# Kernel optimization log

Hardware: AMD Instinct MI355X
Metric: run time of the kernel (lower is better)

The kernel has to match this reference:

```python
import jax, jax.numpy as jnp
from jax import lax
import numpy as np

NUM_TOKENS = 14
DIM = 512
B, T = 32, 512


def _lstm(xs, W_ih, W_hh, b_ih, b_hh):
    """PyTorch-semantics single-layer LSTM, batch_first. xs: [B,T,D] -> hs: [B,T,D].
    Gate order i, f, g, o; gates = x @ W_ih^T + b_ih + h @ W_hh^T + b_hh."""
    Bsz, Tlen, D = xs.shape
    # Precompute input contribution for all timesteps (one big GEMM).
    pre = jnp.einsum('btd,gd->btg', xs, W_ih) + (b_ih + b_hh)  # [B,T,4D]

    def step(carry, p):
        h, c = carry
        gates = p + h @ W_hh.T  # [B,4D]
        i, f, g, o = jnp.split(gates, 4, axis=-1)
        i = jax.nn.sigmoid(i)
        f = jax.nn.sigmoid(f)
        g = jnp.tanh(g)
        o = jax.nn.sigmoid(o)
        c = f * c + i * g
        h = o * jnp.tanh(c)
        return (h, c), h

    h0 = jnp.zeros((Bsz, D), xs.dtype)
    (_, _), hs = lax.scan(step, (h0, h0), jnp.swapaxes(pre, 0, 1))  # time-major scan
    return jnp.swapaxes(hs, 0, 1)  # [B,T,D]


def setup_inputs() -> dict:
    key = jax.random.key(0)
    ks = jax.random.split(key, 10)
    s_emb = 1.0  # nn.Embedding default init N(0,1)
    s = 1.0 / np.sqrt(DIM)  # nn.LSTM default init U(-1/sqrt(H), 1/sqrt(H))
    u = lambda k, shape: jax.random.uniform(k, shape, jnp.float32, -s, s)
    return {
        'x': jax.random.randint(ks[0], (B, T), 0, NUM_TOKENS, dtype=jnp.int32),
        'embed': jax.random.normal(ks[1], (NUM_TOKENS, DIM), jnp.float32) * s_emb,
        'W_ih_q': u(ks[2], (4 * DIM, DIM)),
        'W_hh_q': u(ks[3], (4 * DIM, DIM)),
        'b_ih_q': u(ks[4], (4 * DIM,)),
        'b_hh_q': u(ks[5], (4 * DIM,)),
        'W_ih_k': u(ks[6], (4 * DIM, DIM)),
        'W_hh_k': u(ks[7], (4 * DIM, DIM)),
        'b_ih_k': u(ks[8], (4 * DIM,)),
        'b_hh_k': u(ks[9], (4 * DIM,)),
    }


def reference(x, embed, W_ih_q, W_hh_q, b_ih_q, b_hh_q, W_ih_k, W_hh_k, b_ih_k, b_hh_k):
    e = embed[x]  # [B,T,D] embedding lookup
    q = _lstm(e, W_ih_q, W_hh_q, b_ih_q, b_hh_q)  # [B,T,D]
    k = _lstm(e, W_ih_k, W_hh_k, b_ih_k, b_hh_k)  # [B,T,D]
    A = jnp.einsum('btd,bsd->bts', q, k)  # bmm(q, k^T) -> [B,T,T]
    return A
```

## Files before the change

### kernel.cpp

```cpp
#include <hip/hip_runtime.h>
#include <hip/hip_bf16.h>


#define TB 32
#define TT 512
#define TD 512
#define NTOK 14

typedef __attribute__((ext_vector_type(8))) short short8;
typedef __attribute__((ext_vector_type(4))) float f32x4;

__device__ __forceinline__ float fsigmoid(float v) { return 1.f / (1.f + __expf(-v)); }
__device__ __forceinline__ float ftanh(float v) {
    float a = fabsf(v);
    float e = __expf(-2.f * a);
    float r = (1.f - e) / (1.f + e);
    return copysignf(r, v);
}
__device__ __forceinline__ unsigned int f2bf(float f) {
    __hip_bfloat16 h = __float2bfloat16(f);
    return (unsigned int)__builtin_bit_cast(unsigned short, h);
}

__device__ __forceinline__ short8 load16_coh(const unsigned short* p) {
    short8 r;
    asm volatile("global_load_dwordx4 %0, %1, off sc0 sc1" : "=v"(r) : "v"(p));
    return r;
}
__device__ __forceinline__ void store2_coh(unsigned short* p, unsigned int v) {
    asm volatile("global_store_short %0, %1, off sc0 sc1" :: "v"(p), "v"(v) : "memory");
}
__device__ __forceinline__ void store4_coh(unsigned int* p, unsigned int v) {
    asm volatile("global_store_dword %0, %1, off sc0 sc1" :: "v"(p), "v"(v) : "memory");
}
__device__ __forceinline__ unsigned int load4_coh(const unsigned int* p) {
    unsigned int r;
    asm volatile("global_load_dword %0, %1, off sc0 sc1\n\ts_waitcnt vmcnt(0)"
                 : "=v"(r) : "v"(p) : "memory");
    return r;
}

__global__ __launch_bounds__(256) void pre_tab_kernel(
    const float* __restrict__ embed,
    const float* __restrict__ Wih_q, const float* __restrict__ bih_q, const float* __restrict__ bhh_q,
    const float* __restrict__ Wih_k, const float* __restrict__ bih_k, const float* __restrict__ bhh_k,
    float* __restrict__ pre)
{
    int idx = blockIdx.x * 256 + threadIdx.x;
    int l = idx / (NTOK * 4 * TD);
    int r = idx % (NTOK * 4 * TD);
    int tok = r / (4 * TD), j = r % (4 * TD);
    const float* Wih = l ? Wih_k : Wih_q;
    float acc = l ? (bih_k[j] + bhh_k[j]) : (bih_q[j] + bhh_q[j]);
    const float4* e4 = (const float4*)(embed + (size_t)tok * TD);
    const float4* w4 = (const float4*)(Wih + (size_t)j * TD);
    for (int t2 = 0; t2 < TD / 4; ++t2) {
        float4 e = e4[t2], w = w4[t2];
        acc += e.x * w.x + e.y * w.y + e.z * w.z + e.w * w.w;
    }
    pre[idx] = acc;
}

__global__ void init_flags(unsigned int* flags) { flags[threadIdx.x] = 0; }

__global__ __launch_bounds__(256) void lstm_persist(
    const float* __restrict__ Whh_q, const float* __restrict__ Whh_k,
    const float* __restrict__ pre,
    const int* __restrict__ x,
    float* __restrict__ qout, float* __restrict__ kout,
    unsigned short* __restrict__ hbf,
    unsigned int* __restrict__ flags)
{
    __shared__ unsigned short w_lds[64][512];
    __shared__ unsigned short h_lds[16][512];
    __shared__ float          g_lds[64][17];
    __shared__ unsigned char  x_lds[16 * TT];
    __shared__ float          pre_lds[NTOK][64];

    int wg  = blockIdx.x;
    int l   = wg >> 6;
    int g   = (wg >> 5) & 1;
    int wid = wg & 31;
    int d0  = wid << 4;
    int tid = threadIdx.x;
    int lane = tid & 63;
    int rt  = tid >> 6;

    const float* Whh = l ? Whh_k : Whh_q;
    float* hist = l ? kout : qout;
    unsigned short* hb_l = hbf + (size_t)l * 2 * TB * TD;
    unsigned int* fl = flags + (l * 2 + g) * 32;

    {
        int r = tid >> 2;
        const float* src = Whh + (size_t)((r >> 4) * TD + d0 + (r & 15)) * TD;
#pragma unroll
        for (int i = 0; i < 16; ++i) {
            int c = (tid & 3) + 4 * i;
            float4 a = ((const float4*)src)[c * 2];
            float4 b4 = ((const float4*)src)[c * 2 + 1];
            unsigned short* dst = &w_lds[r][(c ^ (r & 7)) * 8];
            dst[0] = (unsigned short)f2bf(a.x); dst[1] = (unsigned short)f2bf(a.y);
            dst[2] = (unsigned short)f2bf(a.z); dst[3] = (unsigned short)f2bf(a.w);
            dst[4] = (unsigned short)f2bf(b4.x); dst[5] = (unsigned short)f2bf(b4.y);
            dst[6] = (unsigned short)f2bf(b4.z); dst[7] = (unsigned short)f2bf(b4.w);
        }
    }
    for (int i = tid; i < 16 * TT; i += 256)
        x_lds[i] = (unsigned char)x[(g * 16 + (i >> 9)) * TT + (i & 511)];
    for (int i = tid; i < NTOK * 64; i += 256) {
        int tok = i >> 6, j = i & 63;
        pre_lds[tok][j] = pre[((size_t)l * NTOK + tok) * (4 * TD) + (j >> 4) * TD + d0 + (j & 15)];
    }
    __syncthreads();

    int bl = tid >> 4, dd = tid & 15;
    int bg = g * 16 + bl;
    float creg = 0.f;

    {
        int tok = x_lds[bl * TT];
        float i_ = fsigmoid(pre_lds[tok][dd]);
        float f_ = fsigmoid(pre_lds[tok][16 + dd]);
        float g_ = ftanh(pre_lds[tok][32 + dd]);
        float o_ = fsigmoid(pre_lds[tok][48 + dd]);
        creg = i_ * g_;
        float h = o_ * ftanh(creg);
        store2_coh(hb_l + (size_t)bg * TD + d0 + dd, f2bf(h));
        hist[((size_t)bg * TT) * TD + d0 + dd] = h;
        asm volatile("s_waitcnt vmcnt(0)" ::: "memory");
    }
    __syncthreads();
    if (tid == 0) store4_coh(fl + wid, 1u);

    for (int t = 1; t < TT; ++t) {
        {
            unsigned int need = (unsigned int)t;
            for (;;) {
                unsigned int v = load4_coh(fl + (lane & 31));
                if (__all((int)(v >= need))) break;
                __builtin_amdgcn_s_sleep(1);
            }
        }
        {
            int row = tid >> 4;
            const unsigned short* hb = hb_l + (size_t)((t - 1) & 1) * TB * TD
                                            + (size_t)(g * 16 + row) * TD;
            short8 v0 = load16_coh(hb + ((tid & 15) +  0) * 8);
            short8 v1 = load16_coh(hb + ((tid & 15) + 16) * 8);
            short8 v2 = load16_coh(hb + ((tid & 15) + 32) * 8);
            short8 v3 = load16_coh(hb + ((tid & 15) + 48) * 8);
            asm volatile("s_waitcnt vmcnt(0)" ::: "memory");
            __builtin_amdgcn_sched_barrier(0);
            *(short8*)&h_lds[row][(((tid & 15) +  0) ^ (row & 7)) * 8] = v0;
            *(short8*)&h_lds[row][(((tid & 15) + 16) ^ (row & 7)) * 8] = v1;
            *(short8*)&h_lds[row][(((tid & 15) + 32) ^ (row & 7)) * 8] = v2;
            *(short8*)&h_lds[row][(((tid & 15) + 48) ^ (row & 7)) * 8] = v3;
        }
        __syncthreads();

        {
            f32x4 acc = {0.f, 0.f, 0.f, 0.f};
            int rr = rt * 16 + (lane & 15);
            int hr = lane & 15;
#pragma unroll
            for (int kk = 0; kk < 16; ++kk) {
                int c = kk * 4 + (lane >> 4);
                short8 a  = *(const short8*)&h_lds[hr][(c ^ (hr & 7)) * 8];
                short8 bf = *(const short8*)&w_lds[rr][(c ^ (rr & 7)) * 8];
                acc = __builtin_amdgcn_mfma_f32_16x16x32_bf16(a, bf, acc, 0, 0, 0);
            }
            int gb = (lane >> 4) << 2;
#pragma unroll
            for (int r2 = 0; r2 < 4; ++r2) g_lds[rr][gb + r2] = acc[r2];
        }
        __syncthreads();

        {
            int tok = x_lds[bl * TT + t];
            float gi = g_lds[dd][bl]      + pre_lds[tok][dd];
            float gf = g_lds[16 + dd][bl] + pre_lds[tok][16 + dd];
            float gg = g_lds[32 + dd][bl] + pre_lds[tok][32 + dd];
            float go = g_lds[48 + dd][bl] + pre_lds[tok][48 + dd];
            float i_ = fsigmoid(gi), f_ = fsigmoid(gf), g2 = ftanh(gg), o_ = fsigmoid(go);
            creg = f_ * creg + i_ * g2;
            float h = o_ * ftanh(creg);
            store2_coh(hb_l + (size_t)(t & 1) * TB * TD + (size_t)bg * TD + d0 + dd, f2bf(h));
            hist[((size_t)bg * TT + t) * TD + d0 + dd] = h;
            asm volatile("s_waitcnt vmcnt(0)" ::: "memory");
        }
        __syncthreads();
        if (tid == 0) store4_coh(fl + wid, (unsigned int)(t + 1));
    }
}

__global__ __launch_bounds__(256) void qk_gemm(
    const float* __restrict__ q, const float* __restrict__ k, float* __restrict__ A)
{
    __shared__ float qs[64][68];
    __shared__ float ks[64][68];
    int b = blockIdx.y;
    int t0 = (blockIdx.x >> 3) * 64;
    int s0 = (blockIdx.x & 7) * 64;
    const float* qb = q + (size_t)b * TT * TD;
    const float* kb = k + (size_t)b * TT * TD;
    int tid = threadIdx.x;
    int ty = tid >> 4, tx = tid & 15;
    float accr[4][4] = {};
    for (int k0 = 0; k0 < TD; k0 += 64) {
        for (int i = tid; i < 64 * 16; i += 256) {
            int r = i >> 4, c4 = i & 15;
            ((float4*)&qs[r][0])[c4] = ((const float4*)(qb + (size_t)(t0 + r) * TD + k0))[c4];
            ((float4*)&ks[r][0])[c4] = ((const float4*)(kb + (size_t)(s0 + r) * TD + k0))[c4];
        }
        __syncthreads();
#pragma unroll 4
        for (int kk = 0; kk < 64; kk += 4) {
            float4 qv[4], kv[4];
#pragma unroll
            for (int i = 0; i < 4; ++i) qv[i] = *(const float4*)&qs[ty * 4 + i][kk];
#pragma unroll
            for (int j = 0; j < 4; ++j) kv[j] = *(const float4*)&ks[tx * 4 + j][kk];
#pragma unroll
            for (int i = 0; i < 4; ++i)
#pragma unroll
                for (int j = 0; j < 4; ++j)
                    accr[i][j] += qv[i].x * kv[j].x + qv[i].y * kv[j].y
                                + qv[i].z * kv[j].z + qv[i].w * kv[j].w;
        }
        __syncthreads();
    }
    for (int i = 0; i < 4; ++i)
        for (int j = 0; j < 4; ++j)
            A[(size_t)b * TT * TT + (size_t)(t0 + ty * 4 + i) * TT + (s0 + tx * 4 + j)] = accr[i][j];
}

extern "C" void kernel_launch(void* const* d_in, const int* in_sizes, int n_in,
                              void* d_out, int out_size, void* d_ws, size_t ws_size,
                              hipStream_t stream)
{
    const int*   x      = (const int*)d_in[0];
    const float* embed  = (const float*)d_in[1];
    const float* Wih_q  = (const float*)d_in[2];
    const float* Whh_q  = (const float*)d_in[3];
    const float* bih_q  = (const float*)d_in[4];
    const float* bhh_q  = (const float*)d_in[5];
    const float* Wih_k  = (const float*)d_in[6];
    const float* Whh_k  = (const float*)d_in[7];
    const float* bih_k  = (const float*)d_in[8];
    const float* bhh_k  = (const float*)d_in[9];

    float* ws   = (float*)d_ws;
    float* q    = ws;
    float* kbuf = q + (size_t)TB * TT * TD;
    float* pre  = kbuf + (size_t)TB * TT * TD;
    unsigned short* hbf = (unsigned short*)(pre + 2 * NTOK * 4 * TD);
    unsigned int* flags = (unsigned int*)(hbf + 65536);

    init_flags<<<1, 128, 0, stream>>>(flags);
    pre_tab_kernel<<<224, 256, 0, stream>>>(embed, Wih_q, bih_q, bhh_q,
                                            Wih_k, bih_k, bhh_k, pre);
    lstm_persist<<<128, 256, 0, stream>>>(Whh_q, Whh_k, pre, x, q, kbuf, hbf, flags);
    dim3 g2(64, 32);
    qk_gemm<<<g2, 256, 0, stream>>>(q, kbuf, (float*)d_out);
}
```

Baseline: 1.651 ms.

## Interleave two batch halves per workgroup to overlap flag waits with compute

Each persistent LSTM workgroup now handles both 16-row batch halves instead of one, halving the grid to 64 workgroups. The two halves are ping-ponged: while one half's MFMA and gate math run, the h-state loads and flag polling for the other half are in flight. This hides inter-workgroup synchronization latency on the serial recurrence. The cost is twice the per-workgroup compute on the critical path, fewer CUs in use, and more intricate flag ordering that could deadlock or race if wrong.

```diff
diff --git a/kernel.cpp b/kernel.cpp
--- a/kernel.cpp
+++ b/kernel.cpp
@@ -74,12 +74,11 @@
     __shared__ unsigned short w_lds[64][512];
     __shared__ unsigned short h_lds[16][512];
     __shared__ float          g_lds[64][17];
-    __shared__ unsigned char  x_lds[16 * TT];
+    __shared__ unsigned char  x_lds[TB * TT];
     __shared__ float          pre_lds[NTOK][64];
 
     int wg  = blockIdx.x;
-    int l   = wg >> 6;
-    int g   = (wg >> 5) & 1;
+    int l   = wg >> 5;
     int wid = wg & 31;
     int d0  = wid << 4;
     int tid = threadIdx.x;
@@ -89,7 +88,8 @@
     const float* Whh = l ? Whh_k : Whh_q;
     float* hist = l ? kout : qout;
     unsigned short* hb_l = hbf + (size_t)l * 2 * TB * TD;
-    unsigned int* fl = flags + (l * 2 + g) * 32;
+    unsigned int* flA = flags + (l * 2 + 0) * 32;
+    unsigned int* flB = flags + (l * 2 + 1) * 32;
 
     {
         int r = tid >> 2;
@@ -106,8 +106,7 @@
             dst[6] = (unsigned short)f2bf(b4.z); dst[7] = (unsigned short)f2bf(b4.w);
         }
     }
-    for (int i = tid; i < 16 * TT; i += 256)
-        x_lds[i] = (unsigned char)x[(g * 16 + (i >> 9)) * TT + (i & 511)];
+    for (int i = tid; i < TB * TT; i += 256) x_lds[i] = (unsigned char)x[i];
     for (int i = tid; i < NTOK * 64; i += 256) {
         int tok = i >> 6, j = i & 63;
         pre_lds[tok][j] = pre[((size_t)l * NTOK + tok) * (4 * TD) + (j >> 4) * TD + d0 + (j & 15)];
@@ -115,49 +114,72 @@
     __syncthreads();
 
     int bl = tid >> 4, dd = tid & 15;
-    int bg = g * 16 + bl;
-    float creg = 0.f;
+    int row = tid >> 4;
+    float cregA = 0.f, cregB = 0.f;
 
     {
-        int tok = x_lds[bl * TT];
-        float i_ = fsigmoid(pre_lds[tok][dd]);
-        float f_ = fsigmoid(pre_lds[tok][16 + dd]);
-        float g_ = ftanh(pre_lds[tok][32 + dd]);
-        float o_ = fsigmoid(pre_lds[tok][48 + dd]);
-        creg = i_ * g_;
-        float h = o_ * ftanh(creg);
-        store2_coh(hb_l + (size_t)bg * TD + d0 + dd, f2bf(h));
-        hist[((size_t)bg * TT) * TD + d0 + dd] = h;
+        int tokA = x_lds[bl * TT];
+        float iA = fsigmoid(pre_lds[tokA][dd]);
+        float fA = fsigmoid(pre_lds[tokA][16 + dd]);
+        float gA = ftanh(pre_lds[tokA][32 + dd]);
+        float oA = fsigmoid(pre_lds[tokA][48 + dd]);
+        cregA = iA * gA;
+        float hA = oA * ftanh(cregA);
+        store2_coh(hb_l + (size_t)bl * TD + d0 + dd, f2bf(hA));
+        hist[((size_t)bl * TT) * TD + d0 + dd] = hA;
+        int tokB = x_lds[(16 + bl) * TT];
+        float iB = fsigmoid(pre_lds[tokB][dd]);
+        float fB = fsigmoid(pre_lds[tokB][16 + dd]);
+        float gB = ftanh(pre_lds[tokB][32 + dd]);
+        float oB = fsigmoid(pre_lds[tokB][48 + dd]);
+        cregB = iB * gB;
+        float hB = oB * ftanh(cregB);
+        store2_coh(hb_l + (size_t)(16 + bl) * TD + d0 + dd, f2bf(hB));
+        hist[((size_t)(16 + bl) * TT) * TD + d0 + dd] = hB;
         asm volatile("s_waitcnt vmcnt(0)" ::: "memory");
     }
     __syncthreads();
-    if (tid == 0) store4_coh(fl + wid, 1u);
+    if (tid == 0) { store4_coh(flA + wid, 1u); store4_coh(flB + wid, 1u); }
+
+    short8 pA0, pA1, pA2, pA3;
+    {
+        for (;;) {
+            unsigned int v = load4_coh(flA + (lane & 31));
+            if (__all((int)(v >= 1u))) break;
+            __builtin_amdgcn_s_sleep(1);
+        }
+        const unsigned short* hb = hb_l + (size_t)row * TD;
+        pA0 = load16_coh(hb + ((tid & 15) +  0) * 8);
+        pA1 = load16_coh(hb + ((tid & 15) + 16) * 8);
+        pA2 = load16_coh(hb + ((tid & 15) + 32) * 8);
+        pA3 = load16_coh(hb + ((tid & 15) + 48) * 8);
+    }
 
     for (int t = 1; t < TT; ++t) {
+        asm volatile("s_waitcnt vmcnt(0)" ::: "memory");
+        __builtin_amdgcn_sched_barrier(0);
+        *(short8*)&h_lds[row][(((tid & 15) +  0) ^ (row & 7)) * 8] = pA0;
+        *(short8*)&h_lds[row][(((tid & 15) + 16) ^ (row & 7)) * 8] = pA1;
+        *(short8*)&h_lds[row][(((tid & 15) + 32) ^ (row & 7)) * 8] = pA2;
+        *(short8*)&h_lds[row][(((tid & 15) + 48) ^ (row & 7)) * 8] = pA3;
+        __syncthreads();
+        if (tid == 0 && t >= 2) store4_coh(flB + wid, (unsigned int)t);
+
+        short8 pB0, pB1, pB2, pB3;
         {
             unsigned int need = (unsigned int)t;
             for (;;) {
-                unsigned int v = load4_coh(fl + (lane & 31));
+                unsigned int v = load4_coh(flB + (lane & 31));
                 if (__all((int)(v >= need))) break;
                 __builtin_amdgcn_s_sleep(1);
             }
-        }
-        {
-            int row = tid >> 4;
             const unsigned short* hb = hb_l + (size_t)((t - 1) & 1) * TB * TD
-                                            + (size_t)(g * 16 + row) * TD;
-            short8 v0 = load16_coh(hb + ((tid & 15) +  0) * 8);
-            short8 v1 = load16_coh(hb + ((tid & 15) + 16) * 8);
-            short8 v2 = load16_coh(hb + ((tid & 15) + 32) * 8);
-            short8 v3 = load16_coh(hb + ((tid & 15) + 48) * 8);
-            asm volatile("s_waitcnt vmcnt(0)" ::: "memory");
-            __builtin_amdgcn_sched_barrier(0);
-            *(short8*)&h_lds[row][(((tid & 15) +  0) ^ (row & 7)) * 8] = v0;
-            *(short8*)&h_lds[row][(((tid & 15) + 16) ^ (row & 7)) * 8] = v1;
-            *(short8*)&h_lds[row][(((tid & 15) + 32) ^ (row & 7)) * 8] = v2;
-            *(short8*)&h_lds[row][(((tid & 15) + 48) ^ (row & 7)) * 8] = v3;
-        }
-        __syncthreads();
+                                            + (size_t)(16 + row) * TD;
+            pB0 = load16_coh(hb + ((tid & 15) +  0) * 8);
+            pB1 = load16_coh(hb + ((tid & 15) + 16) * 8);
+            pB2 = load16_coh(hb + ((tid & 15) + 32) * 8);
+            pB3 = load16_coh(hb + ((tid & 15) + 48) * 8);
+        }
 
         {
             f32x4 acc = {0.f, 0.f, 0.f, 0.f};
@@ -183,14 +205,64 @@
             float gg = g_lds[32 + dd][bl] + pre_lds[tok][32 + dd];
             float go = g_lds[48 + dd][bl] + pre_lds[tok][48 + dd];
             float i_ = fsigmoid(gi), f_ = fsigmoid(gf), g2 = ftanh(gg), o_ = fsigmoid(go);
-            creg = f_ * creg + i_ * g2;
-            float h = o_ * ftanh(creg);
-            store2_coh(hb_l + (size_t)(t & 1) * TB * TD + (size_t)bg * TD + d0 + dd, f2bf(h));
-            hist[((size_t)bg * TT + t) * TD + d0 + dd] = h;
-            asm volatile("s_waitcnt vmcnt(0)" ::: "memory");
-        }
-        __syncthreads();
-        if (tid == 0) store4_coh(fl + wid, (unsigned int)(t + 1));
+            cregA = f_ * cregA + i_ * g2;
+            float h = o_ * ftanh(cregA);
+            store2_coh(hb_l + (size_t)(t & 1) * TB * TD + (size_t)bl * TD + d0 + dd, f2bf(h));
+            hist[((size_t)bl * TT + t) * TD + d0 + dd] = h;
+        }
+
+        asm volatile("s_waitcnt vmcnt(0)" ::: "memory");
+        __builtin_amdgcn_sched_barrier(0);
+        *(short8*)&h_lds[row][(((tid & 15) +  0) ^ (row & 7)) * 8] = pB0;
+        *(short8*)&h_lds[row][(((tid & 15) + 16) ^ (row & 7)) * 8] = pB1;
+        *(short8*)&h_lds[row][(((tid & 15) + 32) ^ (row & 7)) * 8] = pB2;
+        *(short8*)&h_lds[row][(((tid & 15) + 48) ^ (row & 7)) * 8] = pB3;
+        __syncthreads();
+        if (tid == 0) store4_coh(flA + wid, (unsigned int)(t + 1));
+
+        if (t < TT - 1) {
+            unsigned int need = (unsigned int)(t + 1);
+            for (;;) {
+                unsigned int v = load4_coh(flA + (lane & 31));
+                if (__all((int)(v >= need))) break;
+                __builtin_amdgcn_s_sleep(1);
+            }
+            const unsigned short* hb = hb_l + (size_t)(t & 1) * TB * TD + (size_t)row * TD;
+            pA0 = load16_coh(hb + ((tid & 15) +  0) * 8);
+            pA1 = load16_coh(hb + ((tid & 15) + 16) * 8);
+            pA2 = load16_coh(hb + ((tid & 15) + 32) * 8);
+            pA3 = load16_coh(hb + ((tid & 15) + 48) * 8);
+        }
+
+        {
+            f32x4 acc = {0.f, 0.f, 0.f, 0.f};
+            int rr = rt * 16 + (lane & 15);
+            int hr = lane & 15;
+#pragma unroll
+            for (int kk = 0; kk < 16; ++kk) {
+                int c = kk * 4 + (lane >> 4);
+                short8 a  = *(const short8*)&h_lds[hr][(c ^ (hr & 7)) * 8];
+                short8 bf = *(const short8*)&w_lds[rr][(c ^ (rr & 7)) * 8];
+                acc = __builtin_amdgcn_mfma_f32_16x16x32_bf16(a, bf, acc, 0, 0, 0);
+            }
+            int gb = (lane >> 4) << 2;
+#pragma unroll
+            for (int r2 = 0; r2 < 4; ++r2) g_lds[rr][gb + r2] = acc[r2];
+        }
+        __syncthreads();
+
+        {
+            int tok = x_lds[(16 + bl) * TT + t];
+            float gi = g_lds[dd][bl]      + pre_lds[tok][dd];
+            float gf = g_lds[16 + dd][bl] + pre_lds[tok][16 + dd];
+            float gg = g_lds[32 + dd][bl] + pre_lds[tok][32 + dd];
+            float go = g_lds[48 + dd][bl] + pre_lds[tok][48 + dd];
+            float i_ = fsigmoid(gi), f_ = fsigmoid(gf), g2 = ftanh(gg), o_ = fsigmoid(go);
+            cregB = f_ * cregB + i_ * g2;
+            float h = o_ * ftanh(cregB);
+            store2_coh(hb_l + (size_t)(t & 1) * TB * TD + (size_t)(16 + bl) * TD + d0 + dd, f2bf(h));
+            hist[((size_t)(16 + bl) * TT + t) * TD + d0 + dd] = h;
+        }
     }
 }
 
@@ -260,7 +332,7 @@
     init_flags<<<1, 128, 0, stream>>>(flags);
     pre_tab_kernel<<<224, 256, 0, stream>>>(embed, Wih_q, bih_q, bhh_q,
                                             Wih_k, bih_k, bhh_k, pre);
-    lstm_persist<<<128, 256, 0, stream>>>(Whh_q, Whh_k, pre, x, q, kbuf, hbf, flags);
+    lstm_persist<<<64, 256, 0, stream>>>(Whh_q, Whh_k, pre, x, q, kbuf, hbf, flags);
     dim3 g2(64, 32);
     qk_gemm<<<g2, 256, 0, stream>>>(q, kbuf, (float*)d_out);
 }
```

Result: slower. 2.647 ms (+60.3%).

## Use split-bf16 MFMA for QK^T and store LSTM outputs as hi/lo bf16

Applied to the files above, without the earlier changes.

The LSTM kernel now writes each hidden output as a bf16 high part plus a bf16 residual low part instead of fp32. The final Q·K^T batched GEMM is replaced with an MFMA bf16 kernel that runs three products (hh, hl, lh) to approximate fp32 precision. The aim is to move the scalar-FP32 GEMM onto matrix cores and to reduce the store cost of the history writes inside the serial LSTM loop. The trade-off is dropping the lo*lo term, which gives slightly lower precision than fp32, plus three times the MFMA work per product.

```diff
diff --git a/kernel.cpp b/kernel.cpp
--- a/kernel.cpp
+++ b/kernel.cpp
@@ -17,9 +17,13 @@
     float r = (1.f - e) / (1.f + e);
     return copysignf(r, v);
 }
-__device__ __forceinline__ unsigned int f2bf(float f) {
+__device__ __forceinline__ unsigned short f2bf(float f) {
     __hip_bfloat16 h = __float2bfloat16(f);
-    return (unsigned int)__builtin_bit_cast(unsigned short, h);
+    return __builtin_bit_cast(unsigned short, h);
+}
+__device__ __forceinline__ float bf2f(unsigned short u) {
+    unsigned int x = ((unsigned int)u) << 16;
+    return __builtin_bit_cast(float, x);
 }
 
 __device__ __forceinline__ short8 load16_coh(const unsigned short* p) {
@@ -67,7 +71,8 @@
     const float* __restrict__ Whh_q, const float* __restrict__ Whh_k,
     const float* __restrict__ pre,
     const int* __restrict__ x,
-    float* __restrict__ qout, float* __restrict__ kout,
+    unsigned short* __restrict__ qh, unsigned short* __restrict__ ql,
+    unsigned short* __restrict__ kh, unsigned short* __restrict__ kl,
     unsigned short* __restrict__ hbf,
     unsigned int* __restrict__ flags)
 {
@@ -87,7 +92,8 @@
     int rt  = tid >> 6;
 
     const float* Whh = l ? Whh_k : Whh_q;
-    float* hist = l ? kout : qout;
+    unsigned short* hi_arr = l ? kh : qh;
+    unsigned short* lo_arr = l ? kl : ql;
     unsigned short* hb_l = hbf + (size_t)l * 2 * TB * TD;
     unsigned int* fl = flags + (l * 2 + g) * 32;
 
@@ -100,10 +106,10 @@
             float4 a = ((const float4*)src)[c * 2];
             float4 b4 = ((const float4*)src)[c * 2 + 1];
             unsigned short* dst = &w_lds[r][(c ^ (r & 7)) * 8];
-            dst[0] = (unsigned short)f2bf(a.x); dst[1] = (unsigned short)f2bf(a.y);
-            dst[2] = (unsigned short)f2bf(a.z); dst[3] = (unsigned short)f2bf(a.w);
-            dst[4] = (unsigned short)f2bf(b4.x); dst[5] = (unsigned short)f2bf(b4.y);
-            dst[6] = (unsigned short)f2bf(b4.z); dst[7] = (unsigned short)f2bf(b4.w);
+            dst[0] = f2bf(a.x); dst[1] = f2bf(a.y);
+            dst[2] = f2bf(a.z); dst[3] = f2bf(a.w);
+            dst[4] = f2bf(b4.x); dst[5] = f2bf(b4.y);
+            dst[6] = f2bf(b4.z); dst[7] = f2bf(b4.w);
         }
     }
     for (int i = tid; i < 16 * TT; i += 256)
@@ -126,9 +132,12 @@
         float o_ = fsigmoid(pre_lds[tok][48 + dd]);
         creg = i_ * g_;
         float h = o_ * ftanh(creg);
-        store2_coh(hb_l + (size_t)bg * TD + d0 + dd, f2bf(h));
-        hist[((size_t)bg * TT) * TD + d0 + dd] = h;
+        unsigned short hh = f2bf(h);
+        store2_coh(hb_l + (size_t)bg * TD + d0 + dd, hh);
         asm volatile("s_waitcnt vmcnt(0)" ::: "memory");
+        size_t hoff = ((size_t)bg * TT) * TD + d0 + dd;
+        hi_arr[hoff] = hh;
+        lo_arr[hoff] = f2bf(h - bf2f(hh));
     }
     __syncthreads();
     if (tid == 0) store4_coh(fl + wid, 1u);
@@ -185,54 +194,77 @@
             float i_ = fsigmoid(gi), f_ = fsigmoid(gf), g2 = ftanh(gg), o_ = fsigmoid(go);
             creg = f_ * creg + i_ * g2;
             float h = o_ * ftanh(creg);
-            store2_coh(hb_l + (size_t)(t & 1) * TB * TD + (size_t)bg * TD + d0 + dd, f2bf(h));
-            hist[((size_t)bg * TT + t) * TD + d0 + dd] = h;
+            unsigned short hh = f2bf(h);
+            store2_coh(hb_l + (size_t)(t & 1) * TB * TD + (size_t)bg * TD + d0 + dd, hh);
             asm volatile("s_waitcnt vmcnt(0)" ::: "memory");
+            size_t hoff = ((size_t)bg * TT + t) * TD + d0 + dd;
+            hi_arr[hoff] = hh;
+            lo_arr[hoff] = f2bf(h - bf2f(hh));
         }
         __syncthreads();
         if (tid == 0) store4_coh(fl + wid, (unsigned int)(t + 1));
     }
 }
 
-__global__ __launch_bounds__(256) void qk_gemm(
-    const float* __restrict__ q, const float* __restrict__ k, float* __restrict__ A)
+__global__ __launch_bounds__(256) void qk_mfma(
+    const unsigned short* __restrict__ qh, const unsigned short* __restrict__ ql,
+    const unsigned short* __restrict__ kh, const unsigned short* __restrict__ kl,
+    float* __restrict__ A)
 {
-    __shared__ float qs[64][68];
-    __shared__ float ks[64][68];
-    int b = blockIdx.y;
+    __shared__ unsigned short qh_t[64][64];
+    __shared__ unsigned short ql_t[64][64];
+    __shared__ unsigned short kh_t[64][64];
+    __shared__ unsigned short kl_t[64][64];
+
+    int b  = blockIdx.y;
     int t0 = (blockIdx.x >> 3) * 64;
     int s0 = (blockIdx.x & 7) * 64;
-    const float* qb = q + (size_t)b * TT * TD;
-    const float* kb = k + (size_t)b * TT * TD;
     int tid = threadIdx.x;
-    int ty = tid >> 4, tx = tid & 15;
-    float accr[4][4] = {};
-    for (int k0 = 0; k0 < TD; k0 += 64) {
-        for (int i = tid; i < 64 * 16; i += 256) {
-            int r = i >> 4, c4 = i & 15;
-            ((float4*)&qs[r][0])[c4] = ((const float4*)(qb + (size_t)(t0 + r) * TD + k0))[c4];
-            ((float4*)&ks[r][0])[c4] = ((const float4*)(kb + (size_t)(s0 + r) * TD + k0))[c4];
-        }
-        __syncthreads();
-#pragma unroll 4
-        for (int kk = 0; kk < 64; kk += 4) {
-            float4 qv[4], kv[4];
-#pragma unroll
-            for (int i = 0; i < 4; ++i) qv[i] = *(const float4*)&qs[ty * 4 + i][kk];
-#pragma unroll
-            for (int j = 0; j < 4; ++j) kv[j] = *(const float4*)&ks[tx * 4 + j][kk];
-#pragma unroll
-            for (int i = 0; i < 4; ++i)
-#pragma unroll
-                for (int j = 0; j < 4; ++j)
-                    accr[i][j] += qv[i].x * kv[j].x + qv[i].y * kv[j].y
-                                + qv[i].z * kv[j].z + qv[i].w * kv[j].w;
-        }
-        __syncthreads();
-    }
-    for (int i = 0; i < 4; ++i)
-        for (int j = 0; j < 4; ++j)
-            A[(size_t)b * TT * TT + (size_t)(t0 + ty * 4 + i) * TT + (s0 + tx * 4 + j)] = accr[i][j];
+    int lane = tid & 63;
+    int w = tid >> 6;
+
+    int tq = w * 16 + (lane & 15);
+    f32x4 acc0 = {0,0,0,0}, acc1 = {0,0,0,0}, acc2 = {0,0,0,0}, acc3 = {0,0,0,0};
+
+    for (int kc = 0; kc < 8; ++kc) {
+        for (int i = tid; i < 512; i += 256) {
+            int row = i >> 3, c = i & 7;
+            size_t qoff = ((size_t)b * TT + t0 + row) * TD + kc * 64 + c * 8;
+            size_t koff = ((size_t)b * TT + s0 + row) * TD + kc * 64 + c * 8;
+            int d = (c ^ (row & 7)) * 8;
+            *(short8*)&qh_t[row][d] = *(const short8*)(qh + qoff);
+            *(short8*)&ql_t[row][d] = *(const short8*)(ql + qoff);
+            *(short8*)&kh_t[row][d] = *(const short8*)(kh + koff);
+            *(short8*)&kl_t[row][d] = *(const short8*)(kl + koff);
+        }
+        __syncthreads();
+#pragma unroll
+        for (int kk = 0; kk < 2; ++kk) {
+            int c = kk * 4 + (lane >> 4);
+            short8 ah = *(const short8*)&qh_t[tq][(c ^ (tq & 7)) * 8];
+            short8 al = *(const short8*)&ql_t[tq][(c ^ (tq & 7)) * 8];
+#pragma unroll
+            for (int st = 0; st < 4; ++st) {
+                int sr = st * 16 + (lane & 15);
+                short8 bh = *(const short8*)&kh_t[sr][(c ^ (sr & 7)) * 8];
+                short8 bl = *(const short8*)&kl_t[sr][(c ^ (sr & 7)) * 8];
+                f32x4* acc = (st == 0) ? &acc0 : (st == 1) ? &acc1 : (st == 2) ? &acc2 : &acc3;
+                *acc = __builtin_amdgcn_mfma_f32_16x16x32_bf16(ah, bh, *acc, 0, 0, 0);
+                *acc = __builtin_amdgcn_mfma_f32_16x16x32_bf16(ah, bl, *acc, 0, 0, 0);
+                *acc = __builtin_amdgcn_mfma_f32_16x16x32_bf16(al, bh, *acc, 0, 0, 0);
+            }
+        }
+        __syncthreads();
+    }
+    int m = (lane >> 4) << 2;
+    size_t base = (size_t)b * TT * TT + (size_t)(t0 + w * 16 + m) * TT + s0 + (lane & 15);
+#pragma unroll
+    for (int r2 = 0; r2 < 4; ++r2) {
+        A[base + (size_t)r2 * TT +  0] = acc0[r2];
+        A[base + (size_t)r2 * TT + 16] = acc1[r2];
+        A[base + (size_t)r2 * TT + 32] = acc2[r2];
+        A[base + (size_t)r2 * TT + 48] = acc3[r2];
+    }
 }
 
 extern "C" void kernel_launch(void* const* d_in, const int* in_sizes, int n_in,
@@ -250,17 +282,19 @@
     const float* bih_k  = (const float*)d_in[8];
     const float* bhh_k  = (const float*)d_in[9];
 
-    float* ws   = (float*)d_ws;
-    float* q    = ws;
-    float* kbuf = q + (size_t)TB * TT * TD;
-    float* pre  = kbuf + (size_t)TB * TT * TD;
+    unsigned short* qh = (unsigned short*)d_ws;
+    unsigned short* ql = qh + (size_t)TB * TT * TD;
+    unsigned short* kh = ql + (size_t)TB * TT * TD;
+    unsigned short* kl = kh + (size_t)TB * TT * TD;
+    float* pre = (float*)(kl + (size_t)TB * TT * TD);
     unsigned short* hbf = (unsigned short*)(pre + 2 * NTOK * 4 * TD);
     unsigned int* flags = (unsigned int*)(hbf + 65536);
 
     init_flags<<<1, 128, 0, stream>>>(flags);
     pre_tab_kernel<<<224, 256, 0, stream>>>(embed, Wih_q, bih_q, bhh_q,
                                             Wih_k, bih_k, bhh_k, pre);
-    lstm_persist<<<128, 256, 0, stream>>>(Whh_q, Whh_k, pre, x, q, kbuf, hbf, flags);
+    lstm_persist<<<128, 256, 0, stream>>>(Whh_q, Whh_k, pre, x,
+                                          qh, ql, kh, kl, hbf, flags);
     dim3 g2(64, 32);
-    qk_gemm<<<g2, 256, 0, stream>>>(q, kbuf, (float*)d_out);
-}
+    qk_mfma<<<g2, 256, 0, stream>>>(qh, ql, kh, kl, (float*)d_out);
+}
```

Result: faster. 1.558 ms (-5.7%).
